# Kernel tuning notes

Hardware: AMD Instinct MI355X
Metric: run time of the kernel (lower is better)

## Reference

```python
import jax, jax.numpy as jnp
import numpy as np

N_NODES = 50000
N_EDGES = 800000
D = 128
BN_EPS = 1e-5
AGG_EPS = 1e-6


def setup_inputs() -> dict:
    key = jax.random.key(0)
    ks = jax.random.split(key, 20)
    s = 1.0 / np.sqrt(D)
    def w(k):
        return jax.random.normal(k, (D, D), jnp.float32) * s
    def b(k):
        return jax.random.normal(k, (D,), jnp.float32) * 0.01
    return {
        "x": jax.random.normal(ks[0], (N_NODES, D), jnp.float32),
        "e": jax.random.normal(ks[1], (N_EDGES, D), jnp.float32),
        "edge_index": jax.random.randint(ks[2], (2, N_EDGES), 0, N_NODES, jnp.int32),
        "WA": w(ks[3]), "bA": b(ks[4]),
        "WB": w(ks[5]), "bB": b(ks[6]),
        "WC": w(ks[7]), "bC": b(ks[8]),
        "WD": w(ks[9]), "bD": b(ks[10]),
        "WE": w(ks[11]), "bE": b(ks[12]),
        "gamma_x": jnp.ones((D,), jnp.float32), "beta_x": jnp.zeros((D,), jnp.float32),
        "gamma_e": jnp.ones((D,), jnp.float32), "beta_e": jnp.zeros((D,), jnp.float32),
    }


def _batchnorm(v, gamma, beta):
    # training-mode BatchNorm1d: batch stats, biased variance
    mean = v.mean(axis=0)
    var = v.var(axis=0)
    return gamma * (v - mean) * jax.lax.rsqrt(var + BN_EPS) + beta


def reference(x, e, edge_index, WA, bA, WB, bB, WC, bC, WD, bD, WE, bE,
              gamma_x, beta_x, gamma_e, beta_e):
    n_nodes = x.shape[0]
    src = edge_index[0]  # x_j (source)
    dst = edge_index[1]  # x_i (target), aggregation index

    Ax = x @ WA + bA
    Bx = x @ WB + bB
    Ce = e @ WC + bC
    Dx = x @ WD + bD
    Ex = x @ WE + bE

    # message: gather endpoints, gate
    e_ij = Dx[dst] + Ex[src] + Ce            # [n_edges, D]
    sigma_ij = jax.nn.sigmoid(e_ij)

    # aggregate: scatter-sum numerator & denominator, normalize
    num = jax.ops.segment_sum(sigma_ij * Bx[src], dst, num_segments=n_nodes)
    den = jax.ops.segment_sum(sigma_ij, dst, num_segments=n_nodes)
    aggr = num / (den + AGG_EPS)

    # update + BN + ReLU (dropout=0, residual=False per GraphGym wrapper)
    x_out = jax.nn.relu(_batchnorm(Ax + aggr, gamma_x, beta_x))
    e_out = jax.nn.relu(_batchnorm(e_ij, gamma_e, beta_e))
    return x_out, e_out
```

## Files before the change

### kernel.cpp

```cpp
#include <hip/hip_runtime.h>
#include <stdint.h>

#define DD 128
#define NB_G 2048
#define GE   2048

using f32x4  = __attribute__((ext_vector_type(4))) float;
using bf16x8 = __attribute__((ext_vector_type(8))) short;

__device__ __forceinline__ float bf2f(short u) {
  union { unsigned int i; float f; } c;
  c.i = ((unsigned int)(unsigned short)u) << 16;
  return c.f;
}
__device__ __forceinline__ short f2bf(float f) {
  union { float f; unsigned int i; } c;
  c.f = f;
  unsigned int u = c.i;
  u += 0x7fffu + ((u >> 16) & 1u);
  return (short)(u >> 16);
}

__global__ __launch_bounds__(256) void k_zero(int* __restrict__ p, int n) {
  int i = blockIdx.x * 256 + threadIdx.x;
  if (i < n) p[i] = 0;
}

__global__ __launch_bounds__(256) void k_hist(const int* __restrict__ dst, int* __restrict__ deg, int E) {
  int e = blockIdx.x * 256 + threadIdx.x;
  if (e < E) atomicAdd(&deg[dst[e]], 1);
}

__global__ __launch_bounds__(256) void k_scan1(const int* __restrict__ deg, int* __restrict__ off,
                                               int* __restrict__ totals, int n) {
  __shared__ int sm[256];
  int t = threadIdx.x;
  int i = blockIdx.x * 256 + t;
  int v = (i < n) ? deg[i] : 0;
  sm[t] = v;
  __syncthreads();
  int acc = v;
  #pragma unroll
  for (int d = 1; d < 256; d <<= 1) {
    int add = (t >= d) ? sm[t - d] : 0;
    __syncthreads();
    acc += add;
    sm[t] = acc;
    __syncthreads();
  }
  if (i < n) off[i] = acc - v;
  if (t == 255) totals[blockIdx.x] = acc;
}

__global__ __launch_bounds__(256) void k_scan2(const int* __restrict__ totals, int* __restrict__ boff, int nb) {
  __shared__ int sm[256];
  int t = threadIdx.x;
  int v = (t < nb) ? totals[t] : 0;
  sm[t] = v;
  __syncthreads();
  int acc = v;
  #pragma unroll
  for (int d = 1; d < 256; d <<= 1) {
    int add = (t >= d) ? sm[t - d] : 0;
    __syncthreads();
    acc += add;
    sm[t] = acc;
    __syncthreads();
  }
  boff[t] = acc - v;
}

__global__ __launch_bounds__(256) void k_scan3(int* __restrict__ off, const int* __restrict__ boff,
                                               int* __restrict__ cursor, int n) {
  int i = blockIdx.x * 256 + threadIdx.x;
  if (i < n) {
    int o = off[i] + boff[blockIdx.x];
    off[i] = o;
    cursor[i] = o;
  }
}

__global__ __launch_bounds__(256) void k_fill(const int* __restrict__ dst, const int* __restrict__ src,
                                              int* __restrict__ cursor, int* __restrict__ list,
                                              int* __restrict__ srcS, int* __restrict__ posOf, int E) {
  int e = blockIdx.x * 256 + threadIdx.x;
  if (e < E) {
    int p = atomicAdd(&cursor[dst[e]], 1);
    list[p] = e;
    srcS[p] = src[e];
    posOf[e] = p;
  }
}

__global__ __launch_bounds__(256) void k_prewt5(
    const float* __restrict__ WA, const float* __restrict__ WB, const float* __restrict__ WC,
    const float* __restrict__ WD, const float* __restrict__ WE,
    short* __restrict__ WtA, short* __restrict__ WtB, short* __restrict__ WtC,
    short* __restrict__ WtD, short* __restrict__ WtE) {
  const float* Ws[5] = {WA, WB, WC, WD, WE};
  short* Os[5] = {WtA, WtB, WtC, WtD, WtE};
  const float* W = Ws[blockIdx.x];
  short* O = Os[blockIdx.x];
  int t = threadIdx.x, c = t & 127, h = t >> 7;
  for (int p = 0; p < 8; ++p) {
    int k0 = (h * 8 + p) * 8;
    bf16x8 v;
    #pragma unroll
    for (int j = 0; j < 8; ++j) v[j] = f2bf(W[(size_t)(k0 + j) * DD + c]);
    *(bf16x8*)&O[(size_t)c * DD + k0] = v;
  }
}

__global__ __launch_bounds__(256) void k_nodegemm(
    const float* __restrict__ x,
    const short* __restrict__ WtA, const float* __restrict__ bA,
    const short* __restrict__ WtB, const float* __restrict__ bB,
    const short* __restrict__ WtD, const float* __restrict__ bD,
    const short* __restrict__ WtE, const float* __restrict__ bE,
    short* __restrict__ Axh, short* __restrict__ Bxh,
    short* __restrict__ Dxh, short* __restrict__ Exh, int n) {
  int t = threadIdx.x;
  int w = t >> 6, l = t & 63, lg = l >> 4, lc = l & 15;
  int m0 = blockIdx.x * 64;
  int row = m0 + w * 16 + lc;
  bool valid = row < n;
  int rowc = valid ? row : n - 1;

  const float* xr = x + (size_t)rowc * DD;
  bf16x8 af[4];
  #pragma unroll
  for (int kk = 0; kk < 4; ++kk) {
    float4 a0 = *(const float4*)&xr[kk * 32 + lg * 8];
    float4 a1 = *(const float4*)&xr[kk * 32 + lg * 8 + 4];
    af[kk][0] = f2bf(a0.x); af[kk][1] = f2bf(a0.y); af[kk][2] = f2bf(a0.z); af[kk][3] = f2bf(a0.w);
    af[kk][4] = f2bf(a1.x); af[kk][5] = f2bf(a1.y); af[kk][6] = f2bf(a1.z); af[kk][7] = f2bf(a1.w);
  }

  const short* Wt[4] = {WtA, WtB, WtD, WtE};
  const float* bs[4] = {bA, bB, bD, bE};
  short* Os[4] = {Axh, Bxh, Dxh, Exh};

  #pragma unroll
  for (int mi = 0; mi < 4; ++mi) {
    const short* Wm = Wt[mi];
    f32x4 acc[8] = {};
    #pragma unroll
    for (int kk = 0; kk < 4; ++kk) {
      #pragma unroll
      for (int tt = 0; tt < 8; ++tt) {
        bf16x8 bfv = *(const bf16x8*)&Wm[(size_t)(tt * 16 + lc) * DD + kk * 32 + lg * 8];
        acc[tt] = __builtin_amdgcn_mfma_f32_16x16x32_bf16(bfv, af[kk], acc[tt], 0, 0, 0);
      }
    }
    if (valid) {
      short* O = Os[mi];
      #pragma unroll
      for (int tt = 0; tt < 8; ++tt) {
        int f0 = tt * 16 + lg * 4;
        float4 bc = *(const float4*)&bs[mi][f0];
        short4 o;
        o.x = f2bf(acc[tt][0] + bc.x);
        o.y = f2bf(acc[tt][1] + bc.y);
        o.z = f2bf(acc[tt][2] + bc.z);
        o.w = f2bf(acc[tt][3] + bc.w);
        *(short4*)&O[(size_t)row * DD + f0] = o;
      }
    }
  }
}

__global__ __launch_bounds__(256) void k_edge(
    const float* __restrict__ e, const short* __restrict__ WtC, const float* __restrict__ bC,
    const int* __restrict__ srcI, const int* __restrict__ dstI, const int* __restrict__ posOf,
    const short* __restrict__ Dxh, const short* __restrict__ Exh,
    short* __restrict__ eijS, float* __restrict__ pE, int Etot, int ntiles) {
  __shared__ __align__(16) short lds_wt[32 * 64 * 8];
  __shared__ __align__(16) short es[4][16][136];
  int t = threadIdx.x;
  int w = t >> 6, l = t & 63, lg = l >> 4, lc = l & 15;

  #pragma unroll
  for (int i = 0; i < 8; ++i) {
    int slot = w * 8 + i;
    int tt = slot >> 2, kk = slot & 3;
    bf16x8 v = *(const bf16x8*)&WtC[(size_t)(tt * 16 + lc) * DD + kk * 32 + lg * 8];
    *(bf16x8*)&lds_wt[(slot * 64 + l) * 8] = v;
  }
  __syncthreads();

  float bCv[8];
  #pragma unroll
  for (int tt = 0; tt < 8; ++tt) bCv[tt] = bC[tt * 16 + lc];

  float se[8] = {}, qe[8] = {};

  const int stride = gridDim.x;
  int tile = blockIdx.x;

  float4 e32[8];
  int dnN[4], snN[4], posN[4];

  {
    size_t m0 = (size_t)tile * 64;
    size_t row = m0 + w * 16 + lc;
    if (row >= (size_t)Etot) row = Etot - 1;
    const float* er = e + row * DD;
    #pragma unroll
    for (int kk = 0; kk < 4; ++kk) {
      e32[kk * 2]     = *(const float4*)&er[kk * 32 + lg * 8];
      e32[kk * 2 + 1] = *(const float4*)&er[kk * 32 + lg * 8 + 4];
    }
    #pragma unroll
    for (int z = 0; z < 4; ++z) {
      size_t erow = m0 + w * 16 + z * 4 + lg;
      if (erow >= (size_t)Etot) erow = Etot - 1;
      dnN[z] = dstI[erow]; snN[z] = srcI[erow]; posN[z] = posOf[erow];
    }
  }

  for (; tile < ntiles; tile += stride) {
    int dn[4], sn[4], pos[4];
    #pragma unroll
    for (int z = 0; z < 4; ++z) { dn[z] = dnN[z]; sn[z] = snN[z]; pos[z] = posN[z]; }

    bf16x8 dv[4], sv[4];
    #pragma unroll
    for (int z = 0; z < 4; ++z) {
      dv[z] = *(const bf16x8*)&Dxh[(size_t)dn[z] * DD + lc * 8];
      sv[z] = *(const bf16x8*)&Exh[(size_t)sn[z] * DD + lc * 8];
    }

    bf16x8 af[4];
    #pragma unroll
    for (int kk = 0; kk < 4; ++kk) {
      float4 a0 = e32[kk * 2], a1 = e32[kk * 2 + 1];
      af[kk][0] = f2bf(a0.x); af[kk][1] = f2bf(a0.y); af[kk][2] = f2bf(a0.z); af[kk][3] = f2bf(a0.w);
      af[kk][4] = f2bf(a1.x); af[kk][5] = f2bf(a1.y); af[kk][6] = f2bf(a1.z); af[kk][7] = f2bf(a1.w);
    }

    int nt = tile + stride;
    if (nt < ntiles) {
      size_t m0n = (size_t)nt * 64;
      size_t row = m0n + w * 16 + lc;
      if (row >= (size_t)Etot) row = Etot - 1;
      const float* er = e + row * DD;
      #pragma unroll
      for (int kk = 0; kk < 4; ++kk) {
        e32[kk * 2]     = *(const float4*)&er[kk * 32 + lg * 8];
        e32[kk * 2 + 1] = *(const float4*)&er[kk * 32 + lg * 8 + 4];
      }
      #pragma unroll
      for (int z = 0; z < 4; ++z) {
        size_t erow = m0n + w * 16 + z * 4 + lg;
        if (erow >= (size_t)Etot) erow = Etot - 1;
        dnN[z] = dstI[erow]; snN[z] = srcI[erow]; posN[z] = posOf[erow];
      }
    }

    f32x4 acc[8] = {};
    #pragma unroll
    for (int kk = 0; kk < 4; ++kk) {
      #pragma unroll
      for (int tt = 0; tt < 8; ++tt) {
        bf16x8 bfv = *(const bf16x8*)&lds_wt[((tt * 4 + kk) * 64 + l) * 8];
        acc[tt] = __builtin_amdgcn_mfma_f32_16x16x32_bf16(af[kk], bfv, acc[tt], 0, 0, 0);
      }
    }

    #pragma unroll
    for (int tt = 0; tt < 8; ++tt) {
      int col = tt * 16 + lc;
      #pragma unroll
      for (int j = 0; j < 4; ++j)
        es[w][lg * 4 + j][col] = f2bf(acc[tt][j] + bCv[tt]);
    }
    asm volatile("s_waitcnt lgkmcnt(0)" ::: "memory");
    __builtin_amdgcn_sched_barrier(0);

    size_t m0 = (size_t)tile * 64;
    #pragma unroll
    for (int z = 0; z < 4; ++z) {
      size_t erow = m0 + w * 16 + z * 4 + lg;
      if (erow < (size_t)Etot) {
        int r = z * 4 + lg;
        bf16x8 cv = *(const bf16x8*)&es[w][r][lc * 8];
        bf16x8 o;
        #pragma unroll
        for (int j = 0; j < 8; ++j) {
          float v = bf2f(cv[j]) + bf2f(dv[z][j]) + bf2f(sv[z][j]);
          se[j] += v; qe[j] += v * v;
          o[j] = f2bf(v);
        }
        *(bf16x8*)&eijS[(size_t)pos[z] * DD + lc * 8] = o;
      }
    }
    __builtin_amdgcn_sched_barrier(0);
  }

  #pragma unroll
  for (int j = 0; j < 8; ++j) {
    se[j] += __shfl_xor(se[j], 16); se[j] += __shfl_xor(se[j], 32);
    qe[j] += __shfl_xor(qe[j], 16); qe[j] += __shfl_xor(qe[j], 32);
  }
  if (lg == 0) {
    size_t base = ((size_t)blockIdx.x * 4 + w) * 256;
    #pragma unroll
    for (int j = 0; j < 8; ++j) {
      pE[base + lc * 8 + j] = se[j];
      pE[base + 128 + lc * 8 + j] = qe[j];
    }
  }
}

__device__ __forceinline__ void proc_edge(int id, bf16x8 ev, bf16x8 bv,
                                          const float* su, const float* hu,
                                          float* num, float* den,
                                          float* __restrict__ oute, int fi) {
  float va[8];
  #pragma unroll
  for (int j = 0; j < 8; ++j) {
    float v0 = bf2f(ev[j]);
    va[j] = fmaxf(0.f, v0 * su[j] + hu[j]);
    float g0 = 1.f / (1.f + __expf(-v0));
    num[j] += g0 * bf2f(bv[j]);
    den[j] += g0;
  }
  float4 oa, ob;
  oa.x = va[0]; oa.y = va[1]; oa.z = va[2]; oa.w = va[3];
  ob.x = va[4]; ob.y = va[5]; ob.z = va[6]; ob.w = va[7];
  *(float4*)&oute[(size_t)id * DD + fi * 8] = oa;
  *(float4*)&oute[(size_t)id * DD + fi * 8 + 4] = ob;
}

__global__ __launch_bounds__(256) void k_gather(
    const int* __restrict__ off, const int* __restrict__ deg, const int* __restrict__ list,
    const int* __restrict__ srcS, const short* __restrict__ eijS, const short* __restrict__ Bxh,
    const short* __restrict__ Axh, const float* __restrict__ stE,
    float* __restrict__ outx, float* __restrict__ oute,
    float* __restrict__ pX, int n) {
  int t = threadIdx.x;
  int w = t >> 6, l = t & 63;
  int qw = l >> 4, fi = l & 15;
  int waveId = blockIdx.x * 4 + w;
  const int nwaves = NB_G * 4;

  float su[8], hu[8];
  {
    float4 s0 = *(const float4*)&stE[fi * 8], s1 = *(const float4*)&stE[fi * 8 + 4];
    float4 h0 = *(const float4*)&stE[128 + fi * 8], h1 = *(const float4*)&stE[128 + fi * 8 + 4];
    su[0] = s0.x; su[1] = s0.y; su[2] = s0.z; su[3] = s0.w;
    su[4] = s1.x; su[5] = s1.y; su[6] = s1.z; su[7] = s1.w;
    hu[0] = h0.x; hu[1] = h0.y; hu[2] = h0.z; hu[3] = h0.w;
    hu[4] = h1.x; hu[5] = h1.y; hu[6] = h1.z; hu[7] = h1.w;
  }

  float sx[4] = {}, qx[4] = {};

  for (int node = waveId; node < n; node += nwaves) {
    int start = off[node], dg = deg[node];
    float num[8] = {}, den[8] = {};
    int k = qw;
    for (; k + 12 < dg; k += 16) {
      int p0 = start + k, p1 = p0 + 4, p2 = p0 + 8, p3 = p0 + 12;
      int id0 = list[p0], id1 = list[p1], id2 = list[p2], id3 = list[p3];
      int s0 = srcS[p0], s1 = srcS[p1], s2 = srcS[p2], s3 = srcS[p3];
      bf16x8 e0 = *(const bf16x8*)&eijS[(size_t)p0 * DD + fi * 8];
      bf16x8 e1 = *(const bf16x8*)&eijS[(size_t)p1 * DD + fi * 8];
      bf16x8 e2 = *(const bf16x8*)&eijS[(size_t)p2 * DD + fi * 8];
      bf16x8 e3 = *(const bf16x8*)&eijS[(size_t)p3 * DD + fi * 8];
      bf16x8 b0 = *(const bf16x8*)&Bxh[(size_t)s0 * DD + fi * 8];
      bf16x8 b1 = *(const bf16x8*)&Bxh[(size_t)s1 * DD + fi * 8];
      bf16x8 b2 = *(const bf16x8*)&Bxh[(size_t)s2 * DD + fi * 8];
      bf16x8 b3 = *(const bf16x8*)&Bxh[(size_t)s3 * DD + fi * 8];
      proc_edge(id0, e0, b0, su, hu, num, den, oute, fi);
      proc_edge(id1, e1, b1, su, hu, num, den, oute, fi);
      proc_edge(id2, e2, b2, su, hu, num, den, oute, fi);
      proc_edge(id3, e3, b3, su, hu, num, den, oute, fi);
    }
    for (; k < dg; k += 4) {
      int p0 = start + k;
      int id0 = list[p0];
      int s0 = srcS[p0];
      bf16x8 e0 = *(const bf16x8*)&eijS[(size_t)p0 * DD + fi * 8];
      bf16x8 b0 = *(const bf16x8*)&Bxh[(size_t)s0 * DD + fi * 8];
      proc_edge(id0, e0, b0, su, hu, num, den, oute, fi);
    }
    #pragma unroll
    for (int j = 0; j < 8; ++j) {
      num[j] += __shfl_xor(num[j], 16); num[j] += __shfl_xor(num[j], 32);
      den[j] += __shfl_xor(den[j], 16); den[j] += __shfl_xor(den[j], 32);
    }
    if (qw < 2) {
      int c0 = fi * 8 + qw * 4;
      short4 ax = *(const short4*)&Axh[(size_t)node * DD + c0];
      short axa[4] = {ax.x, ax.y, ax.z, ax.w};
      float4 o;
      float vv[4];
      #pragma unroll
      for (int j = 0; j < 4; ++j) {
        int jj = qw * 4 + j;
        float aggr = num[jj] / (den[jj] + 1e-6f);
        float xp = bf2f(axa[j]) + aggr;
        vv[j] = xp;
        sx[j] += xp; qx[j] += xp * xp;
      }
      o.x = vv[0]; o.y = vv[1]; o.z = vv[2]; o.w = vv[3];
      *(float4*)&outx[(size_t)node * DD + c0] = o;
    }
  }

  __shared__ float lsX[4][128], lqX[4][128];
  if (qw < 2) {
    #pragma unroll
    for (int j = 0; j < 4; ++j) { lsX[w][fi * 8 + qw * 4 + j] = sx[j]; lqX[w][fi * 8 + qw * 4 + j] = qx[j]; }
  }
  __syncthreads();
  if (t < 128) {
    float a = lsX[0][t] + lsX[1][t] + lsX[2][t] + lsX[3][t];
    float b = lqX[0][t] + lqX[1][t] + lqX[2][t] + lqX[3][t];
    pX[(size_t)blockIdx.x * 256 + t] = a;
    pX[(size_t)blockIdx.x * 256 + 128 + t] = b;
  }
}

__global__ __launch_bounds__(256) void k_reduce(const float* __restrict__ part, int nblk, float invcnt,
                                                const float* __restrict__ gamma, const float* __restrict__ beta,
                                                float* __restrict__ stats) {
  int c = blockIdx.x, t = threadIdx.x;
  float a = 0.f, b = 0.f;
  for (int k = t; k < nblk; k += 256) {
    a += part[(size_t)k * 256 + c];
    b += part[(size_t)k * 256 + 128 + c];
  }
  #pragma unroll
  for (int o = 32; o > 0; o >>= 1) { a += __shfl_down(a, o); b += __shfl_down(b, o); }
  __shared__ float ra[4], rb[4];
  int l = t & 63, w = t >> 6;
  if (l == 0) { ra[w] = a; rb[w] = b; }
  __syncthreads();
  if (t == 0) {
    a = ra[0] + ra[1] + ra[2] + ra[3];
    b = rb[0] + rb[1] + rb[2] + rb[3];
    float mean = a * invcnt;
    float var = b * invcnt - mean * mean;
    float istd = rsqrtf(var + 1e-5f);
    float scale = gamma[c] * istd;
    stats[c] = scale;
    stats[128 + c] = beta[c] - mean * scale;
  }
}

__global__ __launch_bounds__(256) void k_xfinal(float* __restrict__ v, const float* __restrict__ st, size_t n4) {
  size_t i = (size_t)blockIdx.x * 256 + threadIdx.x;
  if (i >= n4) return;
  float4 d = *(const float4*)&v[i * 4];
  int f0 = (int)((i * 4) & 127);
  d.x = fmaxf(0.f, d.x * st[f0 + 0] + st[128 + f0 + 0]);
  d.y = fmaxf(0.f, d.y * st[f0 + 1] + st[128 + f0 + 1]);
  d.z = fmaxf(0.f, d.z * st[f0 + 2] + st[128 + f0 + 2]);
  d.w = fmaxf(0.f, d.w * st[f0 + 3] + st[128 + f0 + 3]);
  *(float4*)&v[i * 4] = d;
}

extern "C" void kernel_launch(void* const* d_in, const int* in_sizes, int n_in,
                              void* d_out, int out_size, void* d_ws, size_t ws_size,
                              hipStream_t stream) {
  const float* x  = (const float*)d_in[0];
  const float* e  = (const float*)d_in[1];
  const int*   ei = (const int*)d_in[2];
  const float* WA = (const float*)d_in[3];  const float* bA = (const float*)d_in[4];
  const float* WB = (const float*)d_in[5];  const float* bB = (const float*)d_in[6];
  const float* WC = (const float*)d_in[7];  const float* bC = (const float*)d_in[8];
  const float* WD = (const float*)d_in[9];  const float* bD = (const float*)d_in[10];
  const float* WE = (const float*)d_in[11]; const float* bE = (const float*)d_in[12];
  const float* gx = (const float*)d_in[13]; const float* bx = (const float*)d_in[14];
  const float* ge = (const float*)d_in[15]; const float* be = (const float*)d_in[16];

  int N = in_sizes[0] / DD;
  int E = in_sizes[2] / 2;
  const int* srcI = ei;
  const int* dstI = ei + E;

  float* outx = (float*)d_out;
  float* oute = (float*)d_out + (size_t)N * DD;

  int ntilesE = (E + 63) / 64;

  char* wp = (char*)d_ws;
  auto alloc = [&](size_t sz) { char* p = wp; wp += (sz + 255) & ~(size_t)255; return p; };
  short* Axh    = (short*)alloc((size_t)N * DD * 2);
  short* Bxh    = (short*)alloc((size_t)N * DD * 2);
  short* Dxh    = (short*)alloc((size_t)N * DD * 2);
  short* Exh    = (short*)alloc((size_t)N * DD * 2);
  short* eijS   = (short*)alloc((size_t)E * DD * 2);
  int*   deg    = (int*)alloc((size_t)N * 4);
  int*   off    = (int*)alloc((size_t)N * 4);
  int*   cursor = (int*)alloc((size_t)N * 4);
  int*   totals = (int*)alloc(1024);
  int*   boff   = (int*)alloc(1024);
  int*   list   = (int*)alloc((size_t)E * 4);
  int*   srcS   = (int*)alloc((size_t)E * 4);
  int*   posOf  = (int*)alloc((size_t)E * 4);
  float* pE     = (float*)alloc((size_t)GE * 4 * 256 * 4);
  float* pX     = (float*)alloc((size_t)NB_G * 256 * 4);
  float* statsE = (float*)alloc(1024);
  float* statsX = (float*)alloc(1024);
  short* WtA    = (short*)alloc((size_t)DD * DD * 2);
  short* WtB    = (short*)alloc((size_t)DD * DD * 2);
  short* WtC    = (short*)alloc((size_t)DD * DD * 2);
  short* WtD    = (short*)alloc((size_t)DD * DD * 2);
  short* WtE    = (short*)alloc((size_t)DD * DD * 2);
  (void)ws_size; (void)n_in; (void)out_size;

  int nsb = (N + 255) / 256;

  k_zero<<<nsb, 256, 0, stream>>>(deg, N);
  k_prewt5<<<5, 256, 0, stream>>>(WA, WB, WC, WD, WE, WtA, WtB, WtC, WtD, WtE);
  k_hist<<<(E + 255) / 256, 256, 0, stream>>>(dstI, deg, E);
  k_scan1<<<nsb, 256, 0, stream>>>(deg, off, totals, N);
  k_scan2<<<1, 256, 0, stream>>>(totals, boff, nsb);
  k_scan3<<<nsb, 256, 0, stream>>>(off, boff, cursor, N);
  k_fill<<<(E + 255) / 256, 256, 0, stream>>>(dstI, srcI, cursor, list, srcS, posOf, E);

  k_nodegemm<<<(N + 63) / 64, 256, 0, stream>>>(x, WtA, bA, WtB, bB, WtD, bD, WtE, bE,
                                                Axh, Bxh, Dxh, Exh, N);
  k_edge<<<GE, 256, 0, stream>>>(e, WtC, bC, srcI, dstI, posOf, Dxh, Exh, eijS, pE, E, ntilesE);
  k_reduce<<<128, 256, 0, stream>>>(pE, GE * 4, 1.0f / (float)E, ge, be, statsE);

  k_gather<<<NB_G, 256, 0, stream>>>(off, deg, list, srcS, eijS, Bxh, Axh, statsE,
                                     outx, oute, pX, N);
  k_reduce<<<128, 256, 0, stream>>>(pX, NB_G, 1.0f / (float)N, gx, bx, statsX);
  k_xfinal<<<(int)(((size_t)N * DD / 4 + 255) / 256), 256, 0, stream>>>(outx, statsX, (size_t)N * DD / 4);
}
```

Before: 580.5 us.

## Merge prep kernels, prefetch node offsets, bf16 x intermediate, add 2-edge tail loop

Merges the degree-zeroing and weight-transpose kernels into one launch. In the gather kernel it prefetches the next node's offset and degree, hoists the Axh load ahead of the edge loop, and adds a two-edge unrolled tail. The pre-BatchNorm x output is now staged as bf16 in a workspace buffer and expanded to fp32 in the final kernel, which reduces the intermediate write and read traffic. The cost is an extra rounding of the pre-BN node values to bf16.

```diff
diff --git a/kernel.cpp b/kernel.cpp
--- a/kernel.cpp
+++ b/kernel.cpp
@@ -21,9 +21,30 @@
   return (short)(u >> 16);
 }
 
-__global__ __launch_bounds__(256) void k_zero(int* __restrict__ p, int n) {
-  int i = blockIdx.x * 256 + threadIdx.x;
-  if (i < n) p[i] = 0;
+__global__ __launch_bounds__(256) void k_prep(
+    const float* __restrict__ WA, const float* __restrict__ WB, const float* __restrict__ WC,
+    const float* __restrict__ WD, const float* __restrict__ WE,
+    short* __restrict__ WtA, short* __restrict__ WtB, short* __restrict__ WtC,
+    short* __restrict__ WtD, short* __restrict__ WtE,
+    int* __restrict__ deg, int n) {
+  int t = threadIdx.x;
+  if (blockIdx.x < 5) {
+    const float* Ws[5] = {WA, WB, WC, WD, WE};
+    short* Os[5] = {WtA, WtB, WtC, WtD, WtE};
+    const float* W = Ws[blockIdx.x];
+    short* O = Os[blockIdx.x];
+    int c = t & 127, h = t >> 7;
+    for (int p = 0; p < 8; ++p) {
+      int k0 = (h * 8 + p) * 8;
+      bf16x8 v;
+      #pragma unroll
+      for (int j = 0; j < 8; ++j) v[j] = f2bf(W[(size_t)(k0 + j) * DD + c]);
+      *(bf16x8*)&O[(size_t)c * DD + k0] = v;
+    }
+  } else {
+    int i = (blockIdx.x - 5) * 256 + t;
+    if (i < n) deg[i] = 0;
+  }
 }
 
 __global__ __launch_bounds__(256) void k_hist(const int* __restrict__ dst, int* __restrict__ deg, int E) {
@@ -89,25 +110,6 @@
     list[p] = e;
     srcS[p] = src[e];
     posOf[e] = p;
-  }
-}
-
-__global__ __launch_bounds__(256) void k_prewt5(
-    const float* __restrict__ WA, const float* __restrict__ WB, const float* __restrict__ WC,
-    const float* __restrict__ WD, const float* __restrict__ WE,
-    short* __restrict__ WtA, short* __restrict__ WtB, short* __restrict__ WtC,
-    short* __restrict__ WtD, short* __restrict__ WtE) {
-  const float* Ws[5] = {WA, WB, WC, WD, WE};
-  short* Os[5] = {WtA, WtB, WtC, WtD, WtE};
-  const float* W = Ws[blockIdx.x];
-  short* O = Os[blockIdx.x];
-  int t = threadIdx.x, c = t & 127, h = t >> 7;
-  for (int p = 0; p < 8; ++p) {
-    int k0 = (h * 8 + p) * 8;
-    bf16x8 v;
-    #pragma unroll
-    for (int j = 0; j < 8; ++j) v[j] = f2bf(W[(size_t)(k0 + j) * DD + c]);
-    *(bf16x8*)&O[(size_t)c * DD + k0] = v;
   }
 }
 
@@ -336,7 +338,7 @@
     const int* __restrict__ off, const int* __restrict__ deg, const int* __restrict__ list,
     const int* __restrict__ srcS, const short* __restrict__ eijS, const short* __restrict__ Bxh,
     const short* __restrict__ Axh, const float* __restrict__ stE,
-    float* __restrict__ outx, float* __restrict__ oute,
+    short* __restrict__ outxh, float* __restrict__ oute,
     float* __restrict__ pX, int n) {
   int t = threadIdx.x;
   int w = t >> 6, l = t & 63;
@@ -355,9 +357,17 @@
   }
 
   float sx[4] = {}, qx[4] = {};
+  int c0 = fi * 8 + ((qw & 1) * 4);
+
+  int startC = 0, dgC = 0;
+  if (waveId < n) { startC = off[waveId]; dgC = deg[waveId]; }
 
   for (int node = waveId; node < n; node += nwaves) {
-    int start = off[node], dg = deg[node];
+    int start = startC, dg = dgC;
+    int nn = node + nwaves;
+    if (nn < n) { startC = off[nn]; dgC = deg[nn]; }
+    short4 ax = *(const short4*)&Axh[(size_t)node * DD + (qw < 2 ? c0 : fi * 8)];
+
     float num[8] = {}, den[8] = {};
     int k = qw;
     for (; k + 12 < dg; k += 16) {
@@ -377,6 +387,17 @@
       proc_edge(id2, e2, b2, su, hu, num, den, oute, fi);
       proc_edge(id3, e3, b3, su, hu, num, den, oute, fi);
     }
+    for (; k + 4 < dg; k += 8) {
+      int p0 = start + k, p1 = p0 + 4;
+      int id0 = list[p0], id1 = list[p1];
+      int s0 = srcS[p0], s1 = srcS[p1];
+      bf16x8 e0 = *(const bf16x8*)&eijS[(size_t)p0 * DD + fi * 8];
+      bf16x8 e1 = *(const bf16x8*)&eijS[(size_t)p1 * DD + fi * 8];
+      bf16x8 b0 = *(const bf16x8*)&Bxh[(size_t)s0 * DD + fi * 8];
+      bf16x8 b1 = *(const bf16x8*)&Bxh[(size_t)s1 * DD + fi * 8];
+      proc_edge(id0, e0, b0, su, hu, num, den, oute, fi);
+      proc_edge(id1, e1, b1, su, hu, num, den, oute, fi);
+    }
     for (; k < dg; k += 4) {
       int p0 = start + k;
       int id0 = list[p0];
@@ -391,21 +412,19 @@
       den[j] += __shfl_xor(den[j], 16); den[j] += __shfl_xor(den[j], 32);
     }
     if (qw < 2) {
-      int c0 = fi * 8 + qw * 4;
-      short4 ax = *(const short4*)&Axh[(size_t)node * DD + c0];
       short axa[4] = {ax.x, ax.y, ax.z, ax.w};
-      float4 o;
-      float vv[4];
+      short4 o;
+      short ov[4];
       #pragma unroll
       for (int j = 0; j < 4; ++j) {
         int jj = qw * 4 + j;
         float aggr = num[jj] / (den[jj] + 1e-6f);
         float xp = bf2f(axa[j]) + aggr;
-        vv[j] = xp;
+        ov[j] = f2bf(xp);
         sx[j] += xp; qx[j] += xp * xp;
       }
-      o.x = vv[0]; o.y = vv[1]; o.z = vv[2]; o.w = vv[3];
-      *(float4*)&outx[(size_t)node * DD + c0] = o;
+      o.x = ov[0]; o.y = ov[1]; o.z = ov[2]; o.w = ov[3];
+      *(short4*)&outxh[(size_t)node * DD + c0] = o;
     }
   }
 
@@ -450,16 +469,25 @@
   }
 }
 
-__global__ __launch_bounds__(256) void k_xfinal(float* __restrict__ v, const float* __restrict__ st, size_t n4) {
+__global__ __launch_bounds__(256) void k_xfinal(const short* __restrict__ vh, const float* __restrict__ st,
+                                                float* __restrict__ out, size_t n8) {
   size_t i = (size_t)blockIdx.x * 256 + threadIdx.x;
-  if (i >= n4) return;
-  float4 d = *(const float4*)&v[i * 4];
-  int f0 = (int)((i * 4) & 127);
-  d.x = fmaxf(0.f, d.x * st[f0 + 0] + st[128 + f0 + 0]);
-  d.y = fmaxf(0.f, d.y * st[f0 + 1] + st[128 + f0 + 1]);
-  d.z = fmaxf(0.f, d.z * st[f0 + 2] + st[128 + f0 + 2]);
-  d.w = fmaxf(0.f, d.w * st[f0 + 3] + st[128 + f0 + 3]);
-  *(float4*)&v[i * 4] = d;
+  if (i >= n8) return;
+  bf16x8 u = *(const bf16x8*)&vh[i * 8];
+  int f0 = (int)((i * 8) & 127);
+  float4 s0 = *(const float4*)&st[f0], s1 = *(const float4*)&st[f0 + 4];
+  float4 h0 = *(const float4*)&st[128 + f0], h1 = *(const float4*)&st[128 + f0 + 4];
+  float4 a, b;
+  a.x = fmaxf(0.f, bf2f(u[0]) * s0.x + h0.x);
+  a.y = fmaxf(0.f, bf2f(u[1]) * s0.y + h0.y);
+  a.z = fmaxf(0.f, bf2f(u[2]) * s0.z + h0.z);
+  a.w = fmaxf(0.f, bf2f(u[3]) * s0.w + h0.w);
+  b.x = fmaxf(0.f, bf2f(u[4]) * s1.x + h1.x);
+  b.y = fmaxf(0.f, bf2f(u[5]) * s1.y + h1.y);
+  b.z = fmaxf(0.f, bf2f(u[6]) * s1.z + h1.z);
+  b.w = fmaxf(0.f, bf2f(u[7]) * s1.w + h1.w);
+  *(float4*)&out[i * 8] = a;
+  *(float4*)&out[i * 8 + 4] = b;
 }
 
 extern "C" void kernel_launch(void* const* d_in, const int* in_sizes, int n_in,
@@ -493,6 +521,7 @@
   short* Dxh    = (short*)alloc((size_t)N * DD * 2);
   short* Exh    = (short*)alloc((size_t)N * DD * 2);
   short* eijS   = (short*)alloc((size_t)E * DD * 2);
+  short* outxh  = (short*)alloc((size_t)N * DD * 2);
   int*   deg    = (int*)alloc((size_t)N * 4);
   int*   off    = (int*)alloc((size_t)N * 4);
   int*   cursor = (int*)alloc((size_t)N * 4);
@@ -514,8 +543,7 @@
 
   int nsb = (N + 255) / 256;
 
-  k_zero<<<nsb, 256, 0, stream>>>(deg, N);
-  k_prewt5<<<5, 256, 0, stream>>>(WA, WB, WC, WD, WE, WtA, WtB, WtC, WtD, WtE);
+  k_prep<<<5 + nsb, 256, 0, stream>>>(WA, WB, WC, WD, WE, WtA, WtB, WtC, WtD, WtE, deg, N);
   k_hist<<<(E + 255) / 256, 256, 0, stream>>>(dstI, deg, E);
   k_scan1<<<nsb, 256, 0, stream>>>(deg, off, totals, N);
   k_scan2<<<1, 256, 0, stream>>>(totals, boff, nsb);
@@ -528,7 +556,7 @@
   k_reduce<<<128, 256, 0, stream>>>(pE, GE * 4, 1.0f / (float)E, ge, be, statsE);
 
   k_gather<<<NB_G, 256, 0, stream>>>(off, deg, list, srcS, eijS, Bxh, Axh, statsE,
-                                     outx, oute, pX, N);
+                                     outxh, oute, pX, N);
   k_reduce<<<128, 256, 0, stream>>>(pX, NB_G, 1.0f / (float)N, gx, bx, statsX);
-  k_xfinal<<<(int)(((size_t)N * DD / 4 + 255) / 256), 256, 0, stream>>>(outx, statsX, (size_t)N * DD / 4);
-}
+  k_xfinal<<<(int)(((size_t)N * DD / 8 + 255) / 256), 256, 0, stream>>>(outxh, statsX, outx, (size_t)N * DD / 8);
+}
```

Result: faster. 567.0 us, median of 3 (-2.3%).
